# Kernel optimization log

Hardware: AMD Instinct MI355X
Metric: run time of the kernel (lower is better)

Reference implementation:

```python
import jax, jax.numpy as jnp
import numpy as np

PARENTS = (-1, 0, 0, 0, 1, 2, 3, 4, 5, 6, 7, 8, 9, 9, 9, 12, 13, 14, 16, 17, 18, 19, 20, 21)
NUM_JOINTS = 24
ROT_RANGE = 0.2
SCALE_RANGE = 0.1
CAM_JIT = 0.1
IMG_SIZE = 512.0
EPS = 1e-8


def _rodrigues(axis, angle):
    # axis: [B,3] (will be re-normalized as in the torch code), angle: [B]
    axis = axis / (jnp.linalg.norm(axis, axis=1, keepdims=True) + EPS)
    c = jnp.cos(angle)[:, None, None]
    s = jnp.sin(angle)[:, None, None]
    x, y, z = axis[:, 0], axis[:, 1], axis[:, 2]
    zeros = jnp.zeros_like(x)
    K = jnp.stack([
        jnp.stack([zeros, -z, y], axis=1),
        jnp.stack([z, zeros, -x], axis=1),
        jnp.stack([-y, x, zeros], axis=1),
    ], axis=1)  # [B,3,3]
    I = jnp.eye(3, dtype=axis.dtype)[None]
    outer = axis[:, :, None] * axis[:, None, :]
    return I + s * K + (1.0 - c) * (outer - I)


def setup_inputs() -> dict:
    key = jax.random.key(0)
    ks = jax.random.split(key, 12)
    B, J = 131072, NUM_JOINTS
    return {
        'poses_3d': jax.random.normal(ks[0], (B, J, 3), jnp.float32),
        'rot_mats': jax.random.normal(ks[1], (B, J, 3, 3), jnp.float32),
        'axis': jax.random.normal(ks[2], (B, J, 3), jnp.float32),
        'angle_u': jax.random.uniform(ks[3], (B, J), jnp.float32),
        'scale_u': jax.random.uniform(ks[4], (B, J), jnp.float32),
        'K': jax.random.normal(ks[5], (B, 3, 3), jnp.float32),
        'R': jax.random.normal(ks[6], (B, 3, 3), jnp.float32),
        't': jax.random.normal(ks[7], (B, 3), jnp.float32),
        'focal_u': jax.random.uniform(ks[8], (B, 2), jnp.float32),
        'yaw_u': jax.random.uniform(ks[9], (B,), jnp.float32),
        'pitch_u': jax.random.uniform(ks[10], (B,), jnp.float32),
        't_jit': jax.random.normal(ks[11], (B, 3), jnp.float32),
    }


def reference(poses_3d, rot_mats, axis, angle_u, scale_u, K, R, t, focal_u, yaw_u, pitch_u, t_jit):
    poses = poses_3d
    rots = rot_mats
    # sequential kinematic-tree walk (parents[i] < i, so already-updated parents feed children)
    for i in range(1, NUM_JOINTS):
        p = PARENTS[i]
        bone = poses[:, i] - poses[:, p]                                   # [B,3]
        blen = jnp.linalg.norm(bone, axis=1, keepdims=True)
        ax = axis[:, i]
        ax = ax / (jnp.linalg.norm(ax, axis=1, keepdims=True) + EPS)       # first normalization (forward)
        ang = (angle_u[:, i] * 2.0 - 1.0) * ROT_RANGE
        Ra = _rodrigues(ax, ang)                                           # [B,3,3]
        rb = jnp.einsum('bij,bj->bi', Ra, bone)
        scale = 1.0 + (scale_u[:, i:i + 1] * 2.0 - 1.0) * SCALE_RANGE
        nb = rb * scale * blen / (jnp.linalg.norm(rb, axis=1, keepdims=True) + EPS)
        poses = poses.at[:, i].set(poses[:, p] + nb)
        rots = rots.at[:, i].set(jnp.einsum('bij,bjk->bik', rots[:, i], Ra))

    # camera jitter
    fs = 1.0 + (focal_u * 2.0 - 1.0) * CAM_JIT * 0.1                       # [B,2]
    K_aug = K.at[:, 0, 0].set(K[:, 0, 0] * fs[:, 0]).at[:, 1, 1].set(K[:, 1, 1] * fs[:, 1])
    yaw = (yaw_u * 2.0 - 1.0) * CAM_JIT * 0.1
    pitch = (pitch_u * 2.0 - 1.0) * CAM_JIT * 0.05
    cy, sy = jnp.cos(yaw), jnp.sin(yaw)
    cp, sp = jnp.cos(pitch), jnp.sin(pitch)
    z = jnp.zeros_like(cy)
    o = jnp.ones_like(cy)
    R_yaw = jnp.stack([jnp.stack([cy, z, sy], 1), jnp.stack([z, o, z], 1), jnp.stack([-sy, z, cy], 1)], 1)
    R_pitch = jnp.stack([jnp.stack([o, z, z], 1), jnp.stack([z, cp, -sp], 1), jnp.stack([z, sp, cp], 1)], 1)
    R_aug = jnp.einsum('bij,bjk->bik', R, jnp.einsum('bij,bjk->bik', R_yaw, R_pitch))
    t_aug = t + t_jit * CAM_JIT * 0.05

    # project and normalize
    cam = jnp.einsum('bij,bnj->bni', R_aug, poses) + t_aug[:, None, :]     # [B,J,3]
    zc = jnp.maximum(cam[:, :, 2], 1e-5)
    u = K_aug[:, 0, 0][:, None] * (cam[:, :, 0] / zc) + K_aug[:, 0, 2][:, None]
    v = K_aug[:, 1, 1][:, None] * (cam[:, :, 1] / zc) + K_aug[:, 1, 2][:, None]
    poses_2d = jnp.stack([u, v], axis=2) / IMG_SIZE * 2.0 - 1.0

    return poses, poses_2d, rots, K_aug, R_aug, t_aug
```

## Files before the change

### kernel.cpp

```cpp
#include <hip/hip_runtime.h>

#define NJ 24
#define EPSF 1e-8f

static __device__ __forceinline__ int parent_of(int i) {
    constexpr int P[NJ] = {-1, 0, 0, 0, 1, 2, 3, 4, 5, 6, 7, 8, 9, 9, 9, 12, 13, 14, 16, 17, 18, 19, 20, 21};
    return P[i];
}

static __device__ __forceinline__ void make_Ra(float ax, float ay, float az, float au, float R[9]) {
    float n1 = sqrtf(ax*ax + ay*ay + az*az) + EPSF;
    ax /= n1; ay /= n1; az /= n1;
    float n2 = sqrtf(ax*ax + ay*ay + az*az) + EPSF;
    ax /= n2; ay /= n2; az /= n2;
    float ang = (au * 2.0f - 1.0f) * 0.2f;
    float c = cosf(ang), s = sinf(ang), oc = 1.0f - c;
    R[0] = 1.0f + oc*(ax*ax - 1.0f); R[1] = -s*az + oc*ax*ay;        R[2] =  s*ay + oc*ax*az;
    R[3] =  s*az + oc*ax*ay;         R[4] = 1.0f + oc*(ay*ay - 1.0f); R[5] = -s*ax + oc*ay*az;
    R[6] = -s*ay + oc*ax*az;         R[7] =  s*ax + oc*ay*az;         R[8] = 1.0f + oc*(az*az - 1.0f);
}

__global__ __launch_bounds__(64)
void poseaug_chain_kernel(const float* __restrict__ poses_3d,
                          const float* __restrict__ axis,
                          const float* __restrict__ angle_u,
                          const float* __restrict__ scale_u,
                          const float* __restrict__ Kin,
                          const float* __restrict__ Rin,
                          const float* __restrict__ tin,
                          const float* __restrict__ focal_u,
                          const float* __restrict__ yaw_u,
                          const float* __restrict__ pitch_u,
                          const float* __restrict__ t_jit,
                          float* __restrict__ out, int B)
{
    __shared__ __align__(16) float stg[64 * 73];
    const int l  = threadIdx.x;
    const int e0 = blockIdx.x * 64;
    const int n  = min(64, B - e0);
    const int b  = e0 + l;
    const bool act = (b < B);

    float* out_poses = out;
    float* out_2d    = out + (size_t)B * 72;
    float* out_K     = out + (size_t)B * 336;
    float* out_R     = out + (size_t)B * 345;
    float* out_t     = out + (size_t)B * 354;

    {
        const float* g = poses_3d + (size_t)e0 * 72;
        if (n == 64) {
            const float4* g4 = (const float4*)g;
            #pragma unroll
            for (int it = 0; it < 18; ++it) {
                int i4 = l + it * 64;
                float4 v = g4[i4];
                int o = i4 * 4;
                int base = (o / 72) * 73 + (o % 72);
                stg[base] = v.x; stg[base+1] = v.y; stg[base+2] = v.z; stg[base+3] = v.w;
            }
        } else {
            for (int o = l; o < n * 72; o += 64) stg[(o / 72) * 73 + (o % 72)] = g[o];
        }
    }
    __syncthreads();
    float pf[72];
    #pragma unroll
    for (int k = 0; k < 72; ++k) pf[k] = stg[l * 73 + k];
    __syncthreads();

    {
        const float* g = axis + (size_t)e0 * 72;
        if (n == 64) {
            const float4* g4 = (const float4*)g;
            #pragma unroll
            for (int it = 0; it < 18; ++it) {
                int i4 = l + it * 64;
                float4 v = g4[i4];
                int o = i4 * 4;
                int base = (o / 72) * 73 + (o % 72);
                stg[base] = v.x; stg[base+1] = v.y; stg[base+2] = v.z; stg[base+3] = v.w;
            }
        } else {
            for (int o = l; o < n * 72; o += 64) stg[(o / 72) * 73 + (o % 72)] = g[o];
        }
    }
    __syncthreads();

    float au[24], su[24];
    if (act) {
        const float4* ga = (const float4*)(angle_u + (size_t)b * 24);
        const float4* gs = (const float4*)(scale_u + (size_t)b * 24);
        #pragma unroll
        for (int q = 0; q < 6; ++q) {
            float4 va = ga[q]; au[4*q+0]=va.x; au[4*q+1]=va.y; au[4*q+2]=va.z; au[4*q+3]=va.w;
            float4 vs = gs[q]; su[4*q+0]=vs.x; su[4*q+1]=vs.y; su[4*q+2]=vs.z; su[4*q+3]=vs.w;
        }
    }

    #pragma unroll
    for (int i = 1; i < NJ; ++i) {
        const int par = parent_of(i);
        float bx = pf[3*i+0] - pf[3*par+0];
        float by = pf[3*i+1] - pf[3*par+1];
        float bz = pf[3*i+2] - pf[3*par+2];
        float blen = sqrtf(bx*bx + by*by + bz*bz);

        float Ra[9];
        make_Ra(stg[l*73 + 3*i + 0], stg[l*73 + 3*i + 1], stg[l*73 + 3*i + 2], au[i], Ra);

        float rbx = Ra[0]*bx + Ra[1]*by + Ra[2]*bz;
        float rby = Ra[3]*bx + Ra[4]*by + Ra[5]*bz;
        float rbz = Ra[6]*bx + Ra[7]*by + Ra[8]*bz;

        float scale = 1.0f + (su[i] * 2.0f - 1.0f) * 0.1f;
        float rn = sqrtf(rbx*rbx + rby*rby + rbz*rbz) + EPSF;
        float f = scale * blen / rn;

        pf[3*i+0] = pf[3*par+0] + rbx * f;
        pf[3*i+1] = pf[3*par+1] + rby * f;
        pf[3*i+2] = pf[3*par+2] + rbz * f;
    }

    float K00, K02, K11, K12, Kf[9];
    float A[9], tx = 0.f, ty = 0.f, tz = 0.f;
    if (act) {
        const float* kb = Kin + (size_t)b * 9;
        const float* rb = Rin + (size_t)b * 9;
        #pragma unroll
        for (int k = 0; k < 9; ++k) Kf[k] = kb[k];
        float f0 = focal_u[(size_t)b*2+0], f1 = focal_u[(size_t)b*2+1];
        Kf[0] *= 1.0f + (f0*2.0f - 1.0f) * 0.01f;
        Kf[4] *= 1.0f + (f1*2.0f - 1.0f) * 0.01f;
        K00 = Kf[0]; K02 = Kf[2]; K11 = Kf[4]; K12 = Kf[5];

        float yaw   = (yaw_u[b]   * 2.0f - 1.0f) * 0.01f;
        float pitch = (pitch_u[b] * 2.0f - 1.0f) * 0.005f;
        float cy = cosf(yaw),  sy = sinf(yaw);
        float cp = cosf(pitch), sp = sinf(pitch);
        float M00 = cy,   M01 = sy*sp, M02 = sy*cp;
        float M11 = cp,   M12 = -sp;
        float M20 = -sy,  M21 = cy*sp, M22 = cy*cp;

        float R00=rb[0],R01=rb[1],R02=rb[2],R10=rb[3],R11=rb[4],R12=rb[5],R20=rb[6],R21=rb[7],R22=rb[8];
        A[0] = R00*M00 + R02*M20; A[1] = R00*M01 + R01*M11 + R02*M21; A[2] = R00*M02 + R01*M12 + R02*M22;
        A[3] = R10*M00 + R12*M20; A[4] = R10*M01 + R11*M11 + R12*M21; A[5] = R10*M02 + R11*M12 + R12*M22;
        A[6] = R20*M00 + R22*M20; A[7] = R20*M01 + R21*M11 + R22*M21; A[8] = R20*M02 + R21*M12 + R22*M22;

        tx = tin[(size_t)b*3+0] + t_jit[(size_t)b*3+0] * 0.005f;
        ty = tin[(size_t)b*3+1] + t_jit[(size_t)b*3+1] * 0.005f;
        tz = tin[(size_t)b*3+2] + t_jit[(size_t)b*3+2] * 0.005f;

        float* ok = out_K + (size_t)b * 9;
        #pragma unroll
        for (int k = 0; k < 9; ++k) ok[k] = Kf[k];
        float* orr = out_R + (size_t)b * 9;
        #pragma unroll
        for (int k = 0; k < 9; ++k) orr[k] = A[k];
        float* ot = out_t + (size_t)b * 3;
        ot[0] = tx; ot[1] = ty; ot[2] = tz;
    }

    __syncthreads();
    #pragma unroll
    for (int k = 0; k < 72; ++k) stg[l * 73 + k] = pf[k];
    __syncthreads();
    {
        float* g = out_poses + (size_t)e0 * 72;
        if (n == 64) {
            float4* g4 = (float4*)g;
            #pragma unroll
            for (int it = 0; it < 18; ++it) {
                int i4 = l + it * 64;
                int o = i4 * 4;
                int base = (o / 72) * 73 + (o % 72);
                g4[i4] = make_float4(stg[base], stg[base+1], stg[base+2], stg[base+3]);
            }
        } else {
            for (int o = l; o < n * 72; o += 64) g[o] = stg[(o / 72) * 73 + (o % 72)];
        }
    }

    __syncthreads();
    if (act) {
        #pragma unroll
        for (int j = 0; j < NJ; ++j) {
            float px = pf[3*j+0], py = pf[3*j+1], pz = pf[3*j+2];
            float cx = A[0]*px + A[1]*py + A[2]*pz + tx;
            float cv = A[3]*px + A[4]*py + A[5]*pz + ty;
            float cz = A[6]*px + A[7]*py + A[8]*pz + tz;
            float zc = fmaxf(cz, 1e-5f);
            stg[l*73 + 2*j + 0] = (K00 * (cx / zc) + K02) * (2.0f / 512.0f) - 1.0f;
            stg[l*73 + 2*j + 1] = (K11 * (cv / zc) + K12) * (2.0f / 512.0f) - 1.0f;
        }
    }
    __syncthreads();
    {
        float* g = out_2d + (size_t)e0 * 48;
        if (n == 64) {
            float4* g4 = (float4*)g;
            #pragma unroll
            for (int it = 0; it < 12; ++it) {
                int i4 = l + it * 64;
                int o = i4 * 4;
                int base = (o / 48) * 73 + (o % 48);
                g4[i4] = make_float4(stg[base], stg[base+1], stg[base+2], stg[base+3]);
            }
        } else {
            for (int o = l; o < n * 48; o += 64) g[o] = stg[(o / 48) * 73 + (o % 48)];
        }
    }
}

__global__ __launch_bounds__(256)
void poseaug_rots_kernel(const float* __restrict__ rot_mats,
                         const float* __restrict__ axis,
                         const float* __restrict__ angle_u,
                         float* __restrict__ out_rots, long P)
{
    __shared__ __align__(16) float buf[2304];
    const int tb = threadIdx.x;
    const long T0 = (long)blockIdx.x * 256;
    const int cnt = (int)min((long)256, P - T0);
    const long t = T0 + tb;

    {
        const float* g = rot_mats + 9 * T0;
        if (cnt == 256) {
            const float4* g4 = (const float4*)g;
            float4 v0 = g4[tb];
            float4 v1 = g4[tb + 256];
            *(float4*)&buf[tb * 4]         = v0;
            *(float4*)&buf[(tb + 256) * 4] = v1;
            if (tb < 64) {
                float4 v2 = g4[tb + 512];
                *(float4*)&buf[(tb + 512) * 4] = v2;
            }
        } else {
            for (int o = tb; o < cnt * 9; o += 256) buf[o] = g[o];
        }
    }
    __syncthreads();

    float m[9];
    float r[9];
    bool act = (tb < cnt);
    if (act) {
        #pragma unroll
        for (int k = 0; k < 9; ++k) m[k] = buf[tb * 9 + k];

        int j = (int)(t % 24);
        if (j == 0) {
            #pragma unroll
            for (int k = 0; k < 9; ++k) r[k] = m[k];
        } else {
            float ax = axis[3*t+0], ay = axis[3*t+1], az = axis[3*t+2];
            float Ra[9];
            make_Ra(ax, ay, az, angle_u[t], Ra);
            r[0] = m[0]*Ra[0] + m[1]*Ra[3] + m[2]*Ra[6];
            r[1] = m[0]*Ra[1] + m[1]*Ra[4] + m[2]*Ra[7];
            r[2] = m[0]*Ra[2] + m[1]*Ra[5] + m[2]*Ra[8];
            r[3] = m[3]*Ra[0] + m[4]*Ra[3] + m[5]*Ra[6];
            r[4] = m[3]*Ra[1] + m[4]*Ra[4] + m[5]*Ra[7];
            r[5] = m[3]*Ra[2] + m[4]*Ra[5] + m[5]*Ra[8];
            r[6] = m[6]*Ra[0] + m[7]*Ra[3] + m[8]*Ra[6];
            r[7] = m[6]*Ra[1] + m[7]*Ra[4] + m[8]*Ra[7];
            r[8] = m[6]*Ra[2] + m[7]*Ra[5] + m[8]*Ra[8];
        }
    }
    __syncthreads();
    if (act) {
        #pragma unroll
        for (int k = 0; k < 9; ++k) buf[tb * 9 + k] = r[k];
    }
    __syncthreads();

    {
        float* g = out_rots + 9 * T0;
        if (cnt == 256) {
            float4* g4 = (float4*)g;
            g4[tb]       = *(float4*)&buf[tb * 4];
            g4[tb + 256] = *(float4*)&buf[(tb + 256) * 4];
            if (tb < 64) g4[tb + 512] = *(float4*)&buf[(tb + 512) * 4];
        } else {
            for (int o = tb; o < cnt * 9; o += 256) g[o] = buf[o];
        }
    }
}

extern "C" void kernel_launch(void* const* d_in, const int* in_sizes, int n_in,
                              void* d_out, int out_size, void* d_ws, size_t ws_size,
                              hipStream_t stream) {
    const float* poses_3d = (const float*)d_in[0];
    const float* rot_mats = (const float*)d_in[1];
    const float* axis     = (const float*)d_in[2];
    const float* angle_u  = (const float*)d_in[3];
    const float* scale_u  = (const float*)d_in[4];
    const float* Kin      = (const float*)d_in[5];
    const float* Rin      = (const float*)d_in[6];
    const float* tin      = (const float*)d_in[7];
    const float* focal_u  = (const float*)d_in[8];
    const float* yaw_u    = (const float*)d_in[9];
    const float* pitch_u  = (const float*)d_in[10];
    const float* t_jit    = (const float*)d_in[11];
    float* out = (float*)d_out;

    const int B = in_sizes[9];
    float* out_rots = out + (size_t)B * 120;

    dim3 blk1(64), grd1((B + 63) / 64);
    hipLaunchKernelGGL(poseaug_chain_kernel, grd1, blk1, 0, stream,
                       poses_3d, axis, angle_u, scale_u, Kin, Rin, tin,
                       focal_u, yaw_u, pitch_u, t_jit, out, B);

    const long P = (long)B * NJ;
    dim3 blk2(256), grd2((unsigned)((P + 255) / 256));
    hipLaunchKernelGGL(poseaug_rots_kernel, grd2, blk2, 0, stream,
                       rot_mats, axis, angle_u, out_rots, P);
}
```

Measured before the change: 405.4 us.

## Fuse rotation-matrix update into pose chain kernel, reusing staged axis data

Merges the separate rots kernel into the per-batch chain kernel. The rotation matrices are staged through a second shared buffer in three chunks and multiplied by Rodrigues matrices built from the axis data already in shared memory. This removes a second launch and the re-read of axis and angle_u from global memory. The poses and axis loads are also merged into one pass. In exchange, shared memory per block doubles, there are more barriers, and the rot work now runs on only 64 threads per block, which may reduce occupancy and parallelism.

```diff
diff --git a/kernel.cpp b/kernel.cpp
--- a/kernel.cpp
+++ b/kernel.cpp
@@ -21,7 +21,8 @@
 }
 
 __global__ __launch_bounds__(64)
-void poseaug_chain_kernel(const float* __restrict__ poses_3d,
+void poseaug_fused_kernel(const float* __restrict__ poses_3d,
+                          const float* __restrict__ rot_mats,
                           const float* __restrict__ axis,
                           const float* __restrict__ angle_u,
                           const float* __restrict__ scale_u,
@@ -35,6 +36,7 @@
                           float* __restrict__ out, int B)
 {
     __shared__ __align__(16) float stg[64 * 73];
+    __shared__ __align__(16) float rbuf[64 * 73];
     const int l  = threadIdx.x;
     const int e0 = blockIdx.x * 64;
     const int n  = min(64, B - e0);
@@ -43,49 +45,39 @@
 
     float* out_poses = out;
     float* out_2d    = out + (size_t)B * 72;
+    float* out_rots  = out + (size_t)B * 120;
     float* out_K     = out + (size_t)B * 336;
     float* out_R     = out + (size_t)B * 345;
     float* out_t     = out + (size_t)B * 354;
 
     {
-        const float* g = poses_3d + (size_t)e0 * 72;
-        if (n == 64) {
-            const float4* g4 = (const float4*)g;
+        const float* gp = poses_3d + (size_t)e0 * 72;
+        const float* ga = axis     + (size_t)e0 * 72;
+        if (n == 64) {
+            const float4* gp4 = (const float4*)gp;
+            const float4* ga4 = (const float4*)ga;
             #pragma unroll
             for (int it = 0; it < 18; ++it) {
                 int i4 = l + it * 64;
-                float4 v = g4[i4];
+                float4 vp = gp4[i4];
+                float4 va = ga4[i4];
                 int o = i4 * 4;
                 int base = (o / 72) * 73 + (o % 72);
-                stg[base] = v.x; stg[base+1] = v.y; stg[base+2] = v.z; stg[base+3] = v.w;
-            }
-        } else {
-            for (int o = l; o < n * 72; o += 64) stg[(o / 72) * 73 + (o % 72)] = g[o];
+                rbuf[base] = vp.x; rbuf[base+1] = vp.y; rbuf[base+2] = vp.z; rbuf[base+3] = vp.w;
+                stg[base]  = va.x; stg[base+1]  = va.y; stg[base+2]  = va.z; stg[base+3]  = va.w;
+            }
+        } else {
+            for (int o = l; o < n * 72; o += 64) {
+                int base = (o / 72) * 73 + (o % 72);
+                rbuf[base] = gp[o];
+                stg[base]  = ga[o];
+            }
         }
     }
     __syncthreads();
     float pf[72];
     #pragma unroll
-    for (int k = 0; k < 72; ++k) pf[k] = stg[l * 73 + k];
-    __syncthreads();
-
-    {
-        const float* g = axis + (size_t)e0 * 72;
-        if (n == 64) {
-            const float4* g4 = (const float4*)g;
-            #pragma unroll
-            for (int it = 0; it < 18; ++it) {
-                int i4 = l + it * 64;
-                float4 v = g4[i4];
-                int o = i4 * 4;
-                int base = (o / 72) * 73 + (o % 72);
-                stg[base] = v.x; stg[base+1] = v.y; stg[base+2] = v.z; stg[base+3] = v.w;
-            }
-        } else {
-            for (int o = l; o < n * 72; o += 64) stg[(o / 72) * 73 + (o % 72)] = g[o];
-        }
-    }
-    __syncthreads();
+    for (int k = 0; k < 72; ++k) pf[k] = rbuf[l * 73 + k];
 
     float au[24], su[24];
     if (act) {
@@ -122,9 +114,10 @@
         pf[3*i+2] = pf[3*par+2] + rbz * f;
     }
 
-    float K00, K02, K11, K12, Kf[9];
+    float K00, K02, K11, K12;
     float A[9], tx = 0.f, ty = 0.f, tz = 0.f;
     if (act) {
+        float Kf[9];
         const float* kb = Kin + (size_t)b * 9;
         const float* rb = Rin + (size_t)b * 9;
         #pragma unroll
@@ -159,6 +152,71 @@
         for (int k = 0; k < 9; ++k) orr[k] = A[k];
         float* ot = out_t + (size_t)b * 3;
         ot[0] = tx; ot[1] = ty; ot[2] = tz;
+    }
+
+    #pragma unroll
+    for (int c = 0; c < 3; ++c) {
+        __syncthreads();
+        const float* gld = rot_mats + (size_t)e0 * 216 + 72 * c;
+        if (n == 64) {
+            #pragma unroll
+            for (int it = 0; it < 18; ++it) {
+                int f = it * 64 + l;
+                int r = f / 18;
+                int k = (f % 18) * 4;
+                const float4 v = *(const float4*)(gld + (size_t)r * 216 + k);
+                int base = r * 73 + k;
+                rbuf[base] = v.x; rbuf[base+1] = v.y; rbuf[base+2] = v.z; rbuf[base+3] = v.w;
+            }
+        } else {
+            for (int o = l; o < n * 72; o += 64)
+                rbuf[(o/72)*73 + (o%72)] = gld[(size_t)(o/72)*216 + (o%72)];
+        }
+        __syncthreads();
+        if (act) {
+            #pragma unroll
+            for (int jj = 0; jj < 8; ++jj) {
+                const int j = c * 8 + jj;
+                float m[9];
+                #pragma unroll
+                for (int q = 0; q < 9; ++q) m[q] = rbuf[l*73 + 9*jj + q];
+                float r9[9];
+                if (j == 0) {
+                    #pragma unroll
+                    for (int q = 0; q < 9; ++q) r9[q] = m[q];
+                } else {
+                    float Ra[9];
+                    make_Ra(stg[l*73 + 3*j + 0], stg[l*73 + 3*j + 1], stg[l*73 + 3*j + 2], au[j], Ra);
+                    r9[0] = m[0]*Ra[0] + m[1]*Ra[3] + m[2]*Ra[6];
+                    r9[1] = m[0]*Ra[1] + m[1]*Ra[4] + m[2]*Ra[7];
+                    r9[2] = m[0]*Ra[2] + m[1]*Ra[5] + m[2]*Ra[8];
+                    r9[3] = m[3]*Ra[0] + m[4]*Ra[3] + m[5]*Ra[6];
+                    r9[4] = m[3]*Ra[1] + m[4]*Ra[4] + m[5]*Ra[7];
+                    r9[5] = m[3]*Ra[2] + m[4]*Ra[5] + m[5]*Ra[8];
+                    r9[6] = m[6]*Ra[0] + m[7]*Ra[3] + m[8]*Ra[6];
+                    r9[7] = m[6]*Ra[1] + m[7]*Ra[4] + m[8]*Ra[7];
+                    r9[8] = m[6]*Ra[2] + m[7]*Ra[5] + m[8]*Ra[8];
+                }
+                #pragma unroll
+                for (int q = 0; q < 9; ++q) rbuf[l*73 + 9*jj + q] = r9[q];
+            }
+        }
+        __syncthreads();
+        float* gst = out_rots + (size_t)e0 * 216 + 72 * c;
+        if (n == 64) {
+            #pragma unroll
+            for (int it = 0; it < 18; ++it) {
+                int f = it * 64 + l;
+                int r = f / 18;
+                int k = (f % 18) * 4;
+                int base = r * 73 + k;
+                *(float4*)(gst + (size_t)r * 216 + k) =
+                    make_float4(rbuf[base], rbuf[base+1], rbuf[base+2], rbuf[base+3]);
+            }
+        } else {
+            for (int o = l; o < n * 72; o += 64)
+                gst[(size_t)(o/72)*216 + (o%72)] = rbuf[(o/72)*73 + (o%72)];
+        }
     }
 
     __syncthreads();
@@ -208,82 +266,6 @@
             }
         } else {
             for (int o = l; o < n * 48; o += 64) g[o] = stg[(o / 48) * 73 + (o % 48)];
-        }
-    }
-}
-
-__global__ __launch_bounds__(256)
-void poseaug_rots_kernel(const float* __restrict__ rot_mats,
-                         const float* __restrict__ axis,
-                         const float* __restrict__ angle_u,
-                         float* __restrict__ out_rots, long P)
-{
-    __shared__ __align__(16) float buf[2304];
-    const int tb = threadIdx.x;
-    const long T0 = (long)blockIdx.x * 256;
-    const int cnt = (int)min((long)256, P - T0);
-    const long t = T0 + tb;
-
-    {
-        const float* g = rot_mats + 9 * T0;
-        if (cnt == 256) {
-            const float4* g4 = (const float4*)g;
-            float4 v0 = g4[tb];
-            float4 v1 = g4[tb + 256];
-            *(float4*)&buf[tb * 4]         = v0;
-            *(float4*)&buf[(tb + 256) * 4] = v1;
-            if (tb < 64) {
-                float4 v2 = g4[tb + 512];
-                *(float4*)&buf[(tb + 512) * 4] = v2;
-            }
-        } else {
-            for (int o = tb; o < cnt * 9; o += 256) buf[o] = g[o];
-        }
-    }
-    __syncthreads();
-
-    float m[9];
-    float r[9];
-    bool act = (tb < cnt);
-    if (act) {
-        #pragma unroll
-        for (int k = 0; k < 9; ++k) m[k] = buf[tb * 9 + k];
-
-        int j = (int)(t % 24);
-        if (j == 0) {
-            #pragma unroll
-            for (int k = 0; k < 9; ++k) r[k] = m[k];
-        } else {
-            float ax = axis[3*t+0], ay = axis[3*t+1], az = axis[3*t+2];
-            float Ra[9];
-            make_Ra(ax, ay, az, angle_u[t], Ra);
-            r[0] = m[0]*Ra[0] + m[1]*Ra[3] + m[2]*Ra[6];
-            r[1] = m[0]*Ra[1] + m[1]*Ra[4] + m[2]*Ra[7];
-            r[2] = m[0]*Ra[2] + m[1]*Ra[5] + m[2]*Ra[8];
-            r[3] = m[3]*Ra[0] + m[4]*Ra[3] + m[5]*Ra[6];
-            r[4] = m[3]*Ra[1] + m[4]*Ra[4] + m[5]*Ra[7];
-            r[5] = m[3]*Ra[2] + m[4]*Ra[5] + m[5]*Ra[8];
-            r[6] = m[6]*Ra[0] + m[7]*Ra[3] + m[8]*Ra[6];
-            r[7] = m[6]*Ra[1] + m[7]*Ra[4] + m[8]*Ra[7];
-            r[8] = m[6]*Ra[2] + m[7]*Ra[5] + m[8]*Ra[8];
-        }
-    }
-    __syncthreads();
-    if (act) {
-        #pragma unroll
-        for (int k = 0; k < 9; ++k) buf[tb * 9 + k] = r[k];
-    }
-    __syncthreads();
-
-    {
-        float* g = out_rots + 9 * T0;
-        if (cnt == 256) {
-            float4* g4 = (float4*)g;
-            g4[tb]       = *(float4*)&buf[tb * 4];
-            g4[tb + 256] = *(float4*)&buf[(tb + 256) * 4];
-            if (tb < 64) g4[tb + 512] = *(float4*)&buf[(tb + 512) * 4];
-        } else {
-            for (int o = tb; o < cnt * 9; o += 256) g[o] = buf[o];
         }
     }
 }
@@ -306,15 +288,9 @@
     float* out = (float*)d_out;
 
     const int B = in_sizes[9];
-    float* out_rots = out + (size_t)B * 120;
-
-    dim3 blk1(64), grd1((B + 63) / 64);
-    hipLaunchKernelGGL(poseaug_chain_kernel, grd1, blk1, 0, stream,
-                       poses_3d, axis, angle_u, scale_u, Kin, Rin, tin,
+
+    dim3 blk(64), grd((B + 63) / 64);
+    hipLaunchKernelGGL(poseaug_fused_kernel, grd, blk, 0, stream,
+                       poses_3d, rot_mats, axis, angle_u, scale_u, Kin, Rin, tin,
                        focal_u, yaw_u, pitch_u, t_jit, out, B);
-
-    const long P = (long)B * NJ;
-    dim3 blk2(256), grd2((unsigned)((P + 255) / 256));
-    hipLaunchKernelGGL(poseaug_rots_kernel, grd2, blk2, 0, stream,
-                       rot_mats, axis, angle_u, out_rots, P);
-}
+}
```

Result: slower. 484.8 us (+19.6%).
